# Optimization experiments

Measured on AMD Instinct MI355X. Metric: run time of the kernel, lower is better.

Reference implementation:

```python
import jax, jax.numpy as jnp
import numpy as np

EMBED = 1024
HEADS = 16
HEAD_DIM = EMBED // HEADS
SEQ = 2048
BATCH = 2


def setup_inputs() -> dict:
    key = jax.random.key(0)
    ks = jax.random.split(key, 5)
    s = 1.0 / np.sqrt(EMBED)
    return {
        "x": jax.random.normal(ks[0], (BATCH, SEQ, EMBED), jnp.float32),
        "W_qkv": jax.random.uniform(ks[1], (EMBED, 3 * EMBED), jnp.float32, -s, s),
        "b_qkv": jax.random.uniform(ks[2], (3 * EMBED,), jnp.float32, -s, s),
        "W_out": jax.random.uniform(ks[3], (EMBED, EMBED), jnp.float32, -s, s),
        "b_out": jax.random.uniform(ks[4], (EMBED,), jnp.float32, -s, s),
    }


def reference(x, W_qkv, b_qkv, W_out, b_out):
    B, S, E = x.shape
    qkv = x @ W_qkv + b_qkv                      # [B,S,3E]
    q, k, v = jnp.split(qkv, 3, axis=-1)
    # [B,S,E] -> [B,H,S,D]
    def heads(t):
        return t.reshape(B, S, HEADS, HEAD_DIM).transpose(0, 2, 1, 3)
    q, k, v = heads(q), heads(k), heads(v)
    scores = jnp.einsum("bhid,bhjd->bhij", q, k) / np.sqrt(HEAD_DIM)  # [B,H,S,S]
    causal = jnp.tril(jnp.ones((S, S), bool))
    scores = jnp.where(causal[None, None], scores, -jnp.inf)
    probs = jax.nn.softmax(scores, axis=-1)
    out = jnp.einsum("bhij,bhjd->bhid", probs, v)  # [B,H,S,D]
    out = out.transpose(0, 2, 1, 3).reshape(B, S, E)
    return out @ W_out + b_out
```

## Files before the change

kernel.cpp:

```cpp
#include <hip/hip_runtime.h>
#include <hip/hip_bf16.h>
#include <cstdint>
#include <cstddef>


typedef unsigned short u16;
typedef __attribute__((ext_vector_type(8))) short short8;
typedef __attribute__((ext_vector_type(4))) short short4v;
typedef __attribute__((ext_vector_type(4))) float floatx4;

#define MFMA16(a, b, c) __builtin_amdgcn_mfma_f32_16x16x32_bf16((a), (b), (c), 0, 0, 0)

#if __has_builtin(__builtin_amdgcn_mfma_f32_16x16x16_bf16)
#define PV_MFMA(a, b, c) __builtin_amdgcn_mfma_f32_16x16x16_bf16((a), (b), (c), 0, 0, 0)
#elif __has_builtin(__builtin_amdgcn_mfma_f32_16x16x16bf16_1k)
#define PV_MFMA(a, b, c) __builtin_amdgcn_mfma_f32_16x16x16bf16_1k((a), (b), (c), 0, 0, 0)
#else
static __device__ __forceinline__ floatx4 pv_mfma_asm(short4v a, short4v b, floatx4 c) {
    asm volatile("v_mfma_f32_16x16x16_bf16 %0, %1, %2, %0" : "+v"(c) : "v"(a), "v"(b));
    return c;
}
#define PV_MFMA(a, b, c) pv_mfma_asm((a), (b), (c))
#endif

#if __has_builtin(__builtin_amdgcn_exp2f)
#define EXP2(x) __builtin_amdgcn_exp2f(x)
#else
#define EXP2(x) exp2f(x)
#endif

#define QSCALE 0.18033688011f

static __device__ __forceinline__ u16 f2b(float f) {
    union { float f; uint32_t u; } v; v.f = f;
    return (u16)((v.u + 0x7fffu + ((v.u >> 16) & 1u)) >> 16);
}

static __device__ __forceinline__ uint32_t pkbf(float lo, float hi) {
    union { float f; uint32_t u; } a, b; a.f = lo; b.f = hi;
    return __builtin_amdgcn_perm(b.u + 0x8000u, a.u + 0x8000u, 0x07060302u);
}

static __device__ __forceinline__ void async_cp16(const u16* g, u16* lds_wave_base) {
    __builtin_amdgcn_global_load_lds((__attribute__((address_space(1))) void*)g,
                                     (__attribute__((address_space(3))) void*)lds_wave_base,
                                     16, 0, 0);
}


__global__ __launch_bounds__(256) void k_prep(const float* __restrict__ x,
                                              const float* __restrict__ Wq,
                                              const float* __restrict__ Wo,
                                              u16* __restrict__ xb,
                                              u16* __restrict__ wqkvT,
                                              u16* __restrict__ woutT) {
    int bx = blockIdx.x, tid = threadIdx.x;
    if (bx < 2048) {
        int g = bx * 256 + tid;
        const float4* s = (const float4*)x + (size_t)g * 2;
        float4 f0 = s[0], f1 = s[1];
        uint4 r;
        r.x = pkbf(f0.x, f0.y);
        r.y = pkbf(f0.z, f0.w);
        r.z = pkbf(f1.x, f1.y);
        r.w = pkbf(f1.z, f1.w);
        *(uint4*)(xb + (size_t)g * 8) = r;
        return;
    }
    __shared__ float t[32][33];
    const float* src;
    u16* dst;
    int R, C, b;
    if (bx < 5120) { b = bx - 2048; src = Wq; dst = wqkvT; R = 1024; C = 3072; }
    else           { b = bx - 5120; src = Wo; dst = woutT; R = 1024; C = 1024; }
    int nbx = C >> 5;
    int yq = b / nbx, xq = b - yq * nbx;
    int c0 = xq * 32, r0 = yq * 32;
    int tx = tid & 31, ty = tid >> 5;
#pragma unroll
    for (int i = 0; i < 4; ++i)
        t[ty + i * 8][tx] = src[(size_t)(r0 + ty + i * 8) * C + c0 + tx];
    __syncthreads();
#pragma unroll
    for (int i = 0; i < 4; ++i)
        dst[(size_t)(c0 + ty + i * 8) * R + r0 + tx] = f2b(t[tx][ty + i * 8]);
}


__global__ __launch_bounds__(256, 3) void k_qkv_gemm(const u16* __restrict__ A,
                                                     const u16* __restrict__ Bt,
                                                     const float* __restrict__ bias,
                                                     u16* __restrict__ Qb,
                                                     u16* __restrict__ Kb,
                                                     u16* __restrict__ Vtb) {
    __shared__ __align__(16) u16 As[3][128 * 32];
    __shared__ __align__(16) u16 Bs[3][128 * 32];
    int tid = threadIdx.x;
    int w = tid >> 6, lane = tid & 63, quad = lane >> 4, l16 = lane & 15;
    int wm = w >> 1, wn = w & 1;
    int m0 = blockIdx.y * 128, n0 = blockIdx.x * 128;
    int wb = (tid & ~63) * 8;

    int ra0 = tid >> 2, ca0 = (tid & 3) * 8;
    int ra1 = (256 + tid) >> 2, ca1 = (tid & 3) * 8;
    const u16* A0 = &A[(size_t)(m0 + ra0) * 1024 + ca0];
    const u16* A1 = &A[(size_t)(m0 + ra1) * 1024 + ca1];
    const u16* B0 = &Bt[(size_t)(n0 + ra0) * 1024 + ca0];
    const u16* B1 = &Bt[(size_t)(n0 + ra1) * 1024 + ca1];

    auto stage = [&](int src_kt, int slot) {
        int ko = src_kt * 32;
        async_cp16(A0 + ko, &As[slot][wb]);
        async_cp16(A1 + ko, &As[slot][2048 + wb]);
        async_cp16(B0 + ko, &Bs[slot][wb]);
        async_cp16(B1 + ko, &Bs[slot][2048 + wb]);
    };

    floatx4 acc[4][4] = {};
    stage(0, 0);
    stage(1, 1);

    for (int kt = 0; kt < 32; ++kt) {
        asm volatile("s_waitcnt vmcnt(4)" ::: "memory");
        asm volatile("s_barrier" ::: "memory");
        int jn = kt + 2;
        stage(jn < 32 ? jn : 31, jn % 3);
        int s = kt % 3;
        short8 af[4], bf[4];
#pragma unroll
        for (int mt = 0; mt < 4; ++mt)
            af[mt] = *(const short8*)&As[s][(wm * 64 + mt * 16 + l16) * 32 + quad * 8];
#pragma unroll
        for (int nt = 0; nt < 4; ++nt)
            bf[nt] = *(const short8*)&Bs[s][(wn * 64 + nt * 16 + l16) * 32 + quad * 8];
#pragma unroll
        for (int mt = 0; mt < 4; ++mt)
#pragma unroll
            for (int nt = 0; nt < 4; ++nt)
                acc[mt][nt] = MFMA16(af[mt], bf[nt], acc[mt][nt]);
    }

    int region = n0 >> 10;
    if (region == 2) {
#pragma unroll
        for (int mt = 0; mt < 4; ++mt)
#pragma unroll
            for (int nt = 0; nt < 4; ++nt) {
                int n_abs = n0 + wn * 64 + nt * 16 + l16;
                int e = n_abs & 1023, h = e >> 6, d = e & 63;
                float vb = bias[n_abs];
                int mrow = m0 + wm * 64 + mt * 16 + quad * 4;
                int b = mrow >> 11, s0 = mrow & 2047;
                uint2 val;
                val.x = pkbf(acc[mt][nt][0] + vb, acc[mt][nt][1] + vb);
                val.y = pkbf(acc[mt][nt][2] + vb, acc[mt][nt][3] + vb);
                *(uint2*)&Vtb[((size_t)(b * 16 + h) * 64 + d) * 2048 + s0] = val;
            }
    } else {
        u16* dst = region == 0 ? Qb : Kb;
        float scl = region == 0 ? QSCALE : 1.0f;
#pragma unroll
        for (int mt = 0; mt < 4; ++mt)
#pragma unroll
            for (int nt = 0; nt < 4; ++nt)
#pragma unroll
                for (int r = 0; r < 4; ++r) {
                    int m_abs = m0 + wm * 64 + mt * 16 + quad * 4 + r;
                    int n_abs = n0 + wn * 64 + nt * 16 + l16;
                    float val = (acc[mt][nt][r] + bias[n_abs]) * scl;
                    int e = n_abs & 1023, h = e >> 6, d = e & 63;
                    int b = m_abs >> 11, s = m_abs & 2047;
                    dst[((size_t)(b * 16 + h) * 2048 + s) * 64 + d] = f2b(val);
                }
    }
}


__global__ __launch_bounds__(256, 4) void k_out_gemm(const u16* __restrict__ A,
                                                     const u16* __restrict__ Bt,
                                                     const float* __restrict__ bias,
                                                     float* __restrict__ out) {
    __shared__ __align__(16) u16 As[3][64 * 32];
    __shared__ __align__(16) u16 Bs[3][128 * 32];
    int tid = threadIdx.x;
    int w = tid >> 6, lane = tid & 63, quad = lane >> 4, l16 = lane & 15;
    int wm = w >> 1, wn = w & 1;
    int m0 = blockIdx.y * 64, n0 = blockIdx.x * 128;
    int wb = (tid & ~63) * 8;

    int ra0 = tid >> 2, ca0 = (tid & 3) * 8;
    int ra1 = (256 + tid) >> 2;
    const u16* A0 = &A[(size_t)(m0 + ra0) * 1024 + ca0];
    const u16* B0 = &Bt[(size_t)(n0 + ra0) * 1024 + ca0];
    const u16* B1 = &Bt[(size_t)(n0 + ra1) * 1024 + ca0];

    auto stage = [&](int src_kt, int slot) {
        int ko = src_kt * 32;
        async_cp16(A0 + ko, &As[slot][wb]);
        async_cp16(B0 + ko, &Bs[slot][wb]);
        async_cp16(B1 + ko, &Bs[slot][2048 + wb]);
    };

    floatx4 acc[2][4] = {};
    stage(0, 0);
    stage(1, 1);

    for (int kt = 0; kt < 32; ++kt) {
        asm volatile("s_waitcnt vmcnt(3)" ::: "memory");
        asm volatile("s_barrier" ::: "memory");
        int jn = kt + 2;
        stage(jn < 32 ? jn : 31, jn % 3);
        int s = kt % 3;
        short8 af[2], bf[4];
#pragma unroll
        for (int mt = 0; mt < 2; ++mt)
            af[mt] = *(const short8*)&As[s][(wm * 32 + mt * 16 + l16) * 32 + quad * 8];
#pragma unroll
        for (int nt = 0; nt < 4; ++nt)
            bf[nt] = *(const short8*)&Bs[s][(wn * 64 + nt * 16 + l16) * 32 + quad * 8];
#pragma unroll
        for (int mt = 0; mt < 2; ++mt)
#pragma unroll
            for (int nt = 0; nt < 4; ++nt)
                acc[mt][nt] = MFMA16(af[mt], bf[nt], acc[mt][nt]);
    }

#pragma unroll
    for (int mt = 0; mt < 2; ++mt)
#pragma unroll
        for (int nt = 0; nt < 4; ++nt)
#pragma unroll
            for (int r = 0; r < 4; ++r) {
                int m_abs = m0 + wm * 32 + mt * 16 + quad * 4 + r;
                int n_abs = n0 + wn * 64 + nt * 16 + l16;
                out[(size_t)m_abs * 1024 + n_abs] = acc[mt][nt][r] + bias[n_abs];
            }
}


__global__ __launch_bounds__(256, 2) void k_attn(const u16* __restrict__ Qb,
                                                 const u16* __restrict__ Kb,
                                                 const u16* __restrict__ Vtb,
                                                 u16* __restrict__ attnb) {
    __shared__ __align__(16) u16 KV[4][2][4096];
    int tid = threadIdx.x;
    int w = tid >> 6, lane = tid & 63, quad = lane >> 4, l16 = lane & 15;
    int L = blockIdx.x;
    int bh = ((L & 7) << 2) | ((L >> 3) & 3);
    int idx = (L >> 5) & 15;
    int pr = idx < 8 ? idx : 23 - idx;
    int qta = pr, qtb = 31 - pr;
    const u16* Qp = Qb + (size_t)bh * 131072;
    const u16* Kp = Kb + (size_t)bh * 131072;
    const u16* Vp = Vtb + (size_t)bh * 131072;
    int b = bh >> 4, h = bh & 15;

    int r0 = tid >> 3, c0 = ((tid & 7) ^ (r0 & 7)) * 8;
    int f1 = 256 + tid;
    int r1 = f1 >> 3, c1 = ((f1 & 7) ^ (r1 & 7)) * 8;
    int kOff0 = r0 * 64 + c0, kOff1 = r1 * 64 + c1;
    int vOff0 = r0 * 2048 + c0, vOff1 = r1 * 2048 + c1;
    int wb = (tid & ~63) * 8;

    int qrowa = qta * 64 + w * 16 + l16;
    int qrowb = qtb * 64 + w * 16 + l16;
    short8 qa0 = *(const short8*)&Qp[(size_t)qrowa * 64 + quad * 8];
    short8 qa1 = *(const short8*)&Qp[(size_t)qrowa * 64 + 32 + quad * 8];
    short8 qb0 = *(const short8*)&Qp[(size_t)qrowb * 64 + quad * 8];
    short8 qb1 = *(const short8*)&Qp[(size_t)qrowb * 64 + 32 + quad * 8];

    int n = qtb + 1;

    auto stage = [&](int j) {
        u16* Ks = (u16*)KV[j & 3][0];
        u16* Vs = (u16*)KV[j & 3][1];
        const u16* kp = Kp + (size_t)j * 4096;
        const u16* vp = Vp + (size_t)j * 64;
        async_cp16(kp + kOff0, Ks + wb);
        async_cp16(kp + kOff1, Ks + 2048 + wb);
        async_cp16(vp + vOff0, Vs + wb);
        async_cp16(vp + vOff1, Vs + 2048 + wb);
    };

    floatx4 accA[4] = {}, accB[4] = {};
    float ma = -__builtin_inff(), la = 0.f;
    float mb = -__builtin_inff(), lb = 0.f;
    int sw = l16 & 7;

    stage(0); stage(1); stage(2);

    for (int kt = 0; kt < n; ++kt) {
        asm volatile("s_waitcnt vmcnt(8)" ::: "memory");
        asm volatile("s_barrier" ::: "memory");
        {
            int jn = kt + 3;
            stage(jn < n ? jn : n - 1);
        }
        const u16* Ks = (const u16*)KV[kt & 3][0];
        const u16* Vs = (const u16*)KV[kt & 3][1];

        short8 kfa[4], kfb[4];
#pragma unroll
        for (int nt = 0; nt < 4; ++nt) {
            int rb = (nt * 16 + l16) * 8;
            kfa[nt] = *(const short8*)&Ks[(rb + (quad ^ sw)) * 8];
            kfb[nt] = *(const short8*)&Ks[(rb + ((4 + quad) ^ sw)) * 8];
        }
        short4v vf[4][4];
#pragma unroll
        for (int dt = 0; dt < 4; ++dt) {
            const char* rowb = (const char*)Vs + (dt * 16 + l16) * 128 + (quad & 1) * 8;
#pragma unroll
            for (int nt = 0; nt < 4; ++nt) {
                int chunk = nt * 2 + (quad >> 1);
                vf[nt][dt] = *(const short4v*)(rowb + ((chunk ^ sw) * 16));
            }
        }

        auto tile_step = [&](short8 qf0, short8 qf1, int qt_this, float& mr, float& lr,
                             floatx4* accO) {
            floatx4 sa[4] = {};
#pragma unroll
            for (int nt = 0; nt < 4; ++nt) {
                sa[nt] = MFMA16(kfa[nt], qf0, sa[nt]);
                sa[nt] = MFMA16(kfb[nt], qf1, sa[nt]);
            }
            if (kt == qt_this) {
                int q_abs = qt_this * 64 + w * 16 + l16;
#pragma unroll
                for (int nt = 0; nt < 4; ++nt)
#pragma unroll
                    for (int r = 0; r < 4; ++r)
                        if (kt * 64 + nt * 16 + quad * 4 + r > q_abs)
                            sa[nt][r] = -__builtin_inff();
            }
            float v = sa[0][0];
#pragma unroll
            for (int nt = 0; nt < 4; ++nt)
#pragma unroll
                for (int r = 0; r < 4; ++r) v = fmaxf(v, sa[nt][r]);
            v = fmaxf(v, __shfl_xor(v, 16));
            v = fmaxf(v, __shfl_xor(v, 32));
            float m_new = fmaxf(mr, v);
            float alpha = EXP2(mr - m_new);
            float p[4][4];
            float rs = 0.f;
#pragma unroll
            for (int nt = 0; nt < 4; ++nt)
#pragma unroll
                for (int r = 0; r < 4; ++r) {
                    float e = EXP2(sa[nt][r] - m_new);
                    p[nt][r] = e;
                    rs += e;
                }
            rs += __shfl_xor(rs, 16);
            rs += __shfl_xor(rs, 32);
            lr = lr * alpha + rs;
            mr = m_new;
#pragma unroll
            for (int dt = 0; dt < 4; ++dt)
#pragma unroll
                for (int r = 0; r < 4; ++r) accO[dt][r] *= alpha;
#pragma unroll
            for (int nt = 0; nt < 4; ++nt) {
                union { uint2 u; short4v s; } pf;
                pf.u.x = pkbf(p[nt][0], p[nt][1]);
                pf.u.y = pkbf(p[nt][2], p[nt][3]);
#pragma unroll
                for (int dt = 0; dt < 4; ++dt)
                    accO[dt] = PV_MFMA(vf[nt][dt], pf.s, accO[dt]);
            }
        };

        tile_step(qb0, qb1, qtb, mb, lb, accB);
        if (kt <= qta) tile_step(qa0, qa1, qta, ma, la, accA);
    }

    auto epilogue = [&](int qt_this, float lr, const floatx4* accO) {
        int q_abs = qt_this * 64 + w * 16 + l16;
        float inv = 1.f / lr;
        size_t base = ((size_t)(b * 2048 + q_abs)) * 1024 + h * 64;
#pragma unroll
        for (int dt = 0; dt < 4; ++dt) {
            uint2 val;
            val.x = pkbf(accO[dt][0] * inv, accO[dt][1] * inv);
            val.y = pkbf(accO[dt][2] * inv, accO[dt][3] * inv);
            *(uint2*)&attnb[base + dt * 16 + quad * 4] = val;
        }
    };
    epilogue(qta, la, accA);
    epilogue(qtb, lb, accB);
}


extern "C" void kernel_launch(void* const* d_in, const int* in_sizes, int n_in,
                              void* d_out, int out_size, void* d_ws, size_t ws_size,
                              hipStream_t stream) {
    const float* x     = (const float*)d_in[0];
    const float* W_qkv = (const float*)d_in[1];
    const float* b_qkv = (const float*)d_in[2];
    const float* W_out = (const float*)d_in[3];
    const float* b_out = (const float*)d_in[4];
    float* out = (float*)d_out;

    char* p = (char*)d_ws;
    u16* xb    = (u16*)p; p += (size_t)4096 * 1024 * 2;
    u16* wqkvT = (u16*)p; p += (size_t)3072 * 1024 * 2;
    u16* woutT = (u16*)p; p += (size_t)1024 * 1024 * 2;
    u16* Qb    = (u16*)p; p += (size_t)32 * 2048 * 64 * 2;
    u16* Kb    = (u16*)p; p += (size_t)32 * 2048 * 64 * 2;
    u16* Vtb   = (u16*)p; p += (size_t)32 * 64 * 2048 * 2;
    u16* attnb = xb;

    k_prep<<<6144, 256, 0, stream>>>(x, W_qkv, W_out, xb, wqkvT, woutT);
    k_qkv_gemm<<<dim3(24, 32), 256, 0, stream>>>(xb, wqkvT, b_qkv, Qb, Kb, Vtb);
    k_attn<<<512, 256, 0, stream>>>(Qb, Kb, Vtb, attnb);
    k_out_gemm<<<dim3(8, 64), 256, 0, stream>>>(attnb, woutT, b_out, out);
}
```

Measured before the change: 179.8 us.

## Restructure attention kernel to 32x32x16 MFMA with per-wave query-tile roles

Each wave now owns a 32-row strip of a single query tile (A or B) instead of 16 rows of both tiles. It uses 32x32x16 bf16 MFMA for both QK^T and PV, reading K/V fragments straight from LDS inside the loop. The P fragments are rearranged across lane halves with shuffles so they can feed the PV MFMA. The accumulator rescale is skipped when no row max changes (ballot), and a block-parity flip alternates which waves take the short tile. The aim is fewer MFMA instructions, fewer LDS reads and less softmax bookkeeping per tile. The cost is load imbalance within a block: the waves on the short tile sit idle at barriers while the long-tile waves keep computing.

```diff
diff --git a/kernel.cpp b/kernel.cpp
--- a/kernel.cpp
+++ b/kernel.cpp
@@ -6,22 +6,11 @@
 
 typedef unsigned short u16;
 typedef __attribute__((ext_vector_type(8))) short short8;
-typedef __attribute__((ext_vector_type(4))) short short4v;
 typedef __attribute__((ext_vector_type(4))) float floatx4;
+typedef __attribute__((ext_vector_type(16))) float floatx16;
 
 #define MFMA16(a, b, c) __builtin_amdgcn_mfma_f32_16x16x32_bf16((a), (b), (c), 0, 0, 0)
-
-#if __has_builtin(__builtin_amdgcn_mfma_f32_16x16x16_bf16)
-#define PV_MFMA(a, b, c) __builtin_amdgcn_mfma_f32_16x16x16_bf16((a), (b), (c), 0, 0, 0)
-#elif __has_builtin(__builtin_amdgcn_mfma_f32_16x16x16bf16_1k)
-#define PV_MFMA(a, b, c) __builtin_amdgcn_mfma_f32_16x16x16bf16_1k((a), (b), (c), 0, 0, 0)
-#else
-static __device__ __forceinline__ floatx4 pv_mfma_asm(short4v a, short4v b, floatx4 c) {
-    asm volatile("v_mfma_f32_16x16x16_bf16 %0, %1, %2, %0" : "+v"(c) : "v"(a), "v"(b));
-    return c;
-}
-#define PV_MFMA(a, b, c) pv_mfma_asm((a), (b), (c))
-#endif
+#define MFMA32(a, b, c) __builtin_amdgcn_mfma_f32_32x32x16_bf16((a), (b), (c), 0, 0, 0)
 
 #if __has_builtin(__builtin_amdgcn_exp2f)
 #define EXP2(x) __builtin_amdgcn_exp2f(x)
@@ -30,6 +19,7 @@
 #endif
 
 #define QSCALE 0.18033688011f
+#define NEGINF (-__builtin_inff())
 
 static __device__ __forceinline__ u16 f2b(float f) {
     union { float f; uint32_t u; } v; v.f = f;
@@ -244,7 +234,8 @@
                                                  u16* __restrict__ attnb) {
     __shared__ __align__(16) u16 KV[4][2][4096];
     int tid = threadIdx.x;
-    int w = tid >> 6, lane = tid & 63, quad = lane >> 4, l16 = lane & 15;
+    int w = tid >> 6, lane = tid & 63;
+    int l31 = lane & 31, h5 = lane >> 5;
     int L = blockIdx.x;
     int bh = ((L & 7) << 2) | ((L >> 3) & 3);
     int idx = (L >> 5) & 15;
@@ -255,6 +246,12 @@
     const u16* Vp = Vtb + (size_t)bh * 131072;
     int b = bh >> 4, h = bh & 15;
 
+    int flip = (L >> 8) & 1;
+    int roleA = ((w >> 1) ^ flip) & 1;
+    int strip = w & 1;
+    int myqt = roleA ? qta : qtb;
+    int q_abs = myqt * 64 + strip * 32 + l31;
+
     int r0 = tid >> 3, c0 = ((tid & 7) ^ (r0 & 7)) * 8;
     int f1 = 256 + tid;
     int r1 = f1 >> 3, c1 = ((f1 & 7) ^ (r1 & 7)) * 8;
@@ -262,14 +259,13 @@
     int vOff0 = r0 * 2048 + c0, vOff1 = r1 * 2048 + c1;
     int wb = (tid & ~63) * 8;
 
-    int qrowa = qta * 64 + w * 16 + l16;
-    int qrowb = qtb * 64 + w * 16 + l16;
-    short8 qa0 = *(const short8*)&Qp[(size_t)qrowa * 64 + quad * 8];
-    short8 qa1 = *(const short8*)&Qp[(size_t)qrowa * 64 + 32 + quad * 8];
-    short8 qb0 = *(const short8*)&Qp[(size_t)qrowb * 64 + quad * 8];
-    short8 qb1 = *(const short8*)&Qp[(size_t)qrowb * 64 + 32 + quad * 8];
+    short8 qf[4];
+#pragma unroll
+    for (int ck = 0; ck < 4; ++ck)
+        qf[ck] = *(const short8*)&Qp[(size_t)q_abs * 64 + ck * 16 + h5 * 8];
 
     int n = qtb + 1;
+    int my_n = myqt + 1;
 
     auto stage = [&](int j) {
         u16* Ks = (u16*)KV[j & 3][0];
@@ -282,10 +278,8 @@
         async_cp16(vp + vOff1, Vs + 2048 + wb);
     };
 
-    floatx4 accA[4] = {}, accB[4] = {};
-    float ma = -__builtin_inff(), la = 0.f;
-    float mb = -__builtin_inff(), lb = 0.f;
-    int sw = l16 & 7;
+    floatx16 accO[2] = {};
+    float mr = NEGINF, lr = 0.f;
 
     stage(0); stage(1); stage(2);
 
@@ -296,100 +290,100 @@
             int jn = kt + 3;
             stage(jn < n ? jn : n - 1);
         }
-        const u16* Ks = (const u16*)KV[kt & 3][0];
-        const u16* Vs = (const u16*)KV[kt & 3][1];
-
-        short8 kfa[4], kfb[4];
-#pragma unroll
-        for (int nt = 0; nt < 4; ++nt) {
-            int rb = (nt * 16 + l16) * 8;
-            kfa[nt] = *(const short8*)&Ks[(rb + (quad ^ sw)) * 8];
-            kfb[nt] = *(const short8*)&Ks[(rb + ((4 + quad) ^ sw)) * 8];
-        }
-        short4v vf[4][4];
-#pragma unroll
-        for (int dt = 0; dt < 4; ++dt) {
-            const char* rowb = (const char*)Vs + (dt * 16 + l16) * 128 + (quad & 1) * 8;
-#pragma unroll
-            for (int nt = 0; nt < 4; ++nt) {
-                int chunk = nt * 2 + (quad >> 1);
-                vf[nt][dt] = *(const short4v*)(rowb + ((chunk ^ sw) * 16));
-            }
-        }
-
-        auto tile_step = [&](short8 qf0, short8 qf1, int qt_this, float& mr, float& lr,
-                             floatx4* accO) {
-            floatx4 sa[4] = {};
-#pragma unroll
-            for (int nt = 0; nt < 4; ++nt) {
-                sa[nt] = MFMA16(kfa[nt], qf0, sa[nt]);
-                sa[nt] = MFMA16(kfb[nt], qf1, sa[nt]);
-            }
-            if (kt == qt_this) {
-                int q_abs = qt_this * 64 + w * 16 + l16;
-#pragma unroll
-                for (int nt = 0; nt < 4; ++nt)
-#pragma unroll
-                    for (int r = 0; r < 4; ++r)
-                        if (kt * 64 + nt * 16 + quad * 4 + r > q_abs)
-                            sa[nt][r] = -__builtin_inff();
-            }
-            float v = sa[0][0];
-#pragma unroll
-            for (int nt = 0; nt < 4; ++nt)
-#pragma unroll
-                for (int r = 0; r < 4; ++r) v = fmaxf(v, sa[nt][r]);
-            v = fmaxf(v, __shfl_xor(v, 16));
-            v = fmaxf(v, __shfl_xor(v, 32));
-            float m_new = fmaxf(mr, v);
-            float alpha = EXP2(mr - m_new);
-            float p[4][4];
+        if (kt < my_n) {
+            const u16* Ks = (const u16*)KV[kt & 3][0];
+            const u16* Vs = (const u16*)KV[kt & 3][1];
+
+            floatx16 sa[2];
+            sa[0] = 0.f; sa[1] = 0.f;
+#pragma unroll
+            for (int kh = 0; kh < 2; ++kh) {
+                int row = kh * 32 + l31;
+                int swr = row & 7;
+#pragma unroll
+                for (int ck = 0; ck < 4; ++ck) {
+                    int cc = (ck * 2 + h5) ^ swr;
+                    short8 kf = *(const short8*)&Ks[row * 64 + cc * 8];
+                    sa[kh] = MFMA32(kf, qf[ck], sa[kh]);
+                }
+            }
+            if (kt == myqt) {
+#pragma unroll
+                for (int kh = 0; kh < 2; ++kh)
+#pragma unroll
+                    for (int rg = 0; rg < 16; ++rg) {
+                        int key = kt * 64 + kh * 32 + (rg & 3) + 8 * (rg >> 2) + 4 * h5;
+                        if (key > q_abs) sa[kh][rg] = NEGINF;
+                    }
+            }
+            float mx = NEGINF;
+#pragma unroll
+            for (int kh = 0; kh < 2; ++kh)
+#pragma unroll
+                for (int rg = 0; rg < 16; ++rg) mx = fmaxf(mx, sa[kh][rg]);
+            mx = fmaxf(mx, __shfl_xor(mx, 32));
+            float m_new = fmaxf(mr, mx);
+            if (__ballot(m_new > mr)) {
+                float alpha = EXP2(mr - m_new);
+                lr *= alpha;
+                accO[0] *= alpha;
+                accO[1] *= alpha;
+            }
+            mr = m_new;
+            float p[2][16];
             float rs = 0.f;
 #pragma unroll
-            for (int nt = 0; nt < 4; ++nt)
-#pragma unroll
-                for (int r = 0; r < 4; ++r) {
-                    float e = EXP2(sa[nt][r] - m_new);
-                    p[nt][r] = e;
+            for (int kh = 0; kh < 2; ++kh)
+#pragma unroll
+                for (int rg = 0; rg < 16; ++rg) {
+                    float e = EXP2(sa[kh][rg] - m_new);
+                    p[kh][rg] = e;
                     rs += e;
                 }
-            rs += __shfl_xor(rs, 16);
             rs += __shfl_xor(rs, 32);
-            lr = lr * alpha + rs;
-            mr = m_new;
-#pragma unroll
-            for (int dt = 0; dt < 4; ++dt)
-#pragma unroll
-                for (int r = 0; r < 4; ++r) accO[dt][r] *= alpha;
-#pragma unroll
-            for (int nt = 0; nt < 4; ++nt) {
-                union { uint2 u; short4v s; } pf;
-                pf.u.x = pkbf(p[nt][0], p[nt][1]);
-                pf.u.y = pkbf(p[nt][2], p[nt][3]);
-#pragma unroll
-                for (int dt = 0; dt < 4; ++dt)
-                    accO[dt] = PV_MFMA(vf[nt][dt], pf.s, accO[dt]);
-            }
-        };
-
-        tile_step(qb0, qb1, qtb, mb, lb, accB);
-        if (kt <= qta) tile_step(qa0, qa1, qta, ma, la, accA);
+            lr += rs;
+            uint32_t pk[2][8];
+#pragma unroll
+            for (int kh = 0; kh < 2; ++kh)
+#pragma unroll
+                for (int g = 0; g < 8; ++g)
+                    pk[kh][g] = pkbf(p[kh][2 * g], p[kh][2 * g + 1]);
+#pragma unroll
+            for (int kb = 0; kb < 4; ++kb) {
+                int hh = kb >> 1;
+                int base = 4 * (kb & 1);
+                uint32_t o0 = pk[hh][base + 2 * h5];
+                uint32_t o1 = pk[hh][base + 2 * h5 + 1];
+                uint32_t s0 = pk[hh][base + 2 * (1 - h5)];
+                uint32_t s1 = pk[hh][base + 2 * (1 - h5) + 1];
+                uint32_t e0 = (uint32_t)__shfl_xor((int)s0, 32);
+                uint32_t e1 = (uint32_t)__shfl_xor((int)s1, 32);
+                union { uint32_t u[4]; short8 v; } pf;
+                pf.u[0] = h5 ? e0 : o0;
+                pf.u[1] = h5 ? e1 : o1;
+                pf.u[2] = h5 ? o0 : e0;
+                pf.u[3] = h5 ? o1 : e1;
+#pragma unroll
+                for (int dh = 0; dh < 2; ++dh) {
+                    int vrow = dh * 32 + l31;
+                    int cc = (kb * 2 + h5) ^ (vrow & 7);
+                    short8 vf = *(const short8*)&Vs[vrow * 64 + cc * 8];
+                    accO[dh] = MFMA32(vf, pf.v, accO[dh]);
+                }
+            }
+        }
     }
 
-    auto epilogue = [&](int qt_this, float lr, const floatx4* accO) {
-        int q_abs = qt_this * 64 + w * 16 + l16;
-        float inv = 1.f / lr;
-        size_t base = ((size_t)(b * 2048 + q_abs)) * 1024 + h * 64;
-#pragma unroll
-        for (int dt = 0; dt < 4; ++dt) {
-            uint2 val;
-            val.x = pkbf(accO[dt][0] * inv, accO[dt][1] * inv);
-            val.y = pkbf(accO[dt][2] * inv, accO[dt][3] * inv);
-            *(uint2*)&attnb[base + dt * 16 + quad * 4] = val;
+    float inv = 1.f / lr;
+    size_t obase = ((size_t)(b * 2048 + q_abs)) * 1024 + h * 64;
+#pragma unroll
+    for (int dh = 0; dh < 2; ++dh)
+#pragma unroll
+        for (int g = 0; g < 8; ++g) {
+            int d0 = dh * 32 + 2 * (g & 1) + 8 * (g >> 1) + 4 * h5;
+            uint32_t v = pkbf(accO[dh][2 * g] * inv, accO[dh][2 * g + 1] * inv);
+            *(uint32_t*)&attnb[obase + d0] = v;
         }
-    };
-    epilogue(qta, la, accA);
-    epilogue(qtb, lb, accB);
 }
 
 
```

After: 227.2 us. 26.4% more time.

## Assign adjacent query tile pairs per attention block instead of mirrored pairs

Applied to the files above, without the earlier changes.

Each attention block now processes two adjacent 64-row query tiles (2*tile and 2*tile+1) instead of a mirrored pair (pr, 31-pr). Both query tiles share almost the same causal key/value range, so the block streams fewer K/V tiles per query tile and reuses each staged tile for two score computations. The trade-off is losing the load balance of the mirrored pairing: per-block work now grows linearly with the tile index, so the longest blocks do nearly twice the tile steps of the old balanced blocks.

```diff
diff --git a/kernel.cpp b/kernel.cpp
--- a/kernel.cpp
+++ b/kernel.cpp
@@ -30,6 +30,7 @@
 #endif
 
 #define QSCALE 0.18033688011f
+#define NEGINF (-__builtin_inff())
 
 static __device__ __forceinline__ u16 f2b(float f) {
     union { float f; uint32_t u; } v; v.f = f;
@@ -248,8 +249,7 @@
     int L = blockIdx.x;
     int bh = ((L & 7) << 2) | ((L >> 3) & 3);
     int idx = (L >> 5) & 15;
-    int pr = idx < 8 ? idx : 23 - idx;
-    int qta = pr, qtb = 31 - pr;
+    int tile = idx < 8 ? idx : 23 - idx;
     const u16* Qp = Qb + (size_t)bh * 131072;
     const u16* Kp = Kb + (size_t)bh * 131072;
     const u16* Vp = Vtb + (size_t)bh * 131072;
@@ -262,14 +262,14 @@
     int vOff0 = r0 * 2048 + c0, vOff1 = r1 * 2048 + c1;
     int wb = (tid & ~63) * 8;
 
-    int qrowa = qta * 64 + w * 16 + l16;
-    int qrowb = qtb * 64 + w * 16 + l16;
-    short8 qa0 = *(const short8*)&Qp[(size_t)qrowa * 64 + quad * 8];
-    short8 qa1 = *(const short8*)&Qp[(size_t)qrowa * 64 + 32 + quad * 8];
-    short8 qb0 = *(const short8*)&Qp[(size_t)qrowb * 64 + quad * 8];
-    short8 qb1 = *(const short8*)&Qp[(size_t)qrowb * 64 + 32 + quad * 8];
-
-    int n = qtb + 1;
+    int q_s0 = tile * 128 + w * 16 + l16;
+    int q_s1 = q_s0 + 64;
+    short8 q00 = *(const short8*)&Qp[(size_t)q_s0 * 64 + quad * 8];
+    short8 q01 = *(const short8*)&Qp[(size_t)q_s0 * 64 + 32 + quad * 8];
+    short8 q10 = *(const short8*)&Qp[(size_t)q_s1 * 64 + quad * 8];
+    short8 q11 = *(const short8*)&Qp[(size_t)q_s1 * 64 + 32 + quad * 8];
+
+    int n = 2 * tile + 2;
 
     auto stage = [&](int j) {
         u16* Ks = (u16*)KV[j & 3][0];
@@ -282,9 +282,9 @@
         async_cp16(vp + vOff1, Vs + 2048 + wb);
     };
 
-    floatx4 accA[4] = {}, accB[4] = {};
-    float ma = -__builtin_inff(), la = 0.f;
-    float mb = -__builtin_inff(), lb = 0.f;
+    floatx4 acc0[4] = {}, acc1[4] = {};
+    float m0 = NEGINF, l0 = 0.f;
+    float m1 = NEGINF, l1 = 0.f;
     int sw = l16 & 7;
 
     stage(0); stage(1); stage(2);
@@ -317,22 +317,21 @@
             }
         }
 
-        auto tile_step = [&](short8 qf0, short8 qf1, int qt_this, float& mr, float& lr,
-                             floatx4* accO) {
+        auto tile_step = [&](short8 qf0, short8 qf1, int q_abs, bool diag, float& mr,
+                             float& lr, floatx4* accO) {
             floatx4 sa[4] = {};
 #pragma unroll
             for (int nt = 0; nt < 4; ++nt) {
                 sa[nt] = MFMA16(kfa[nt], qf0, sa[nt]);
                 sa[nt] = MFMA16(kfb[nt], qf1, sa[nt]);
             }
-            if (kt == qt_this) {
-                int q_abs = qt_this * 64 + w * 16 + l16;
+            if (diag) {
 #pragma unroll
                 for (int nt = 0; nt < 4; ++nt)
 #pragma unroll
                     for (int r = 0; r < 4; ++r)
                         if (kt * 64 + nt * 16 + quad * 4 + r > q_abs)
-                            sa[nt][r] = -__builtin_inff();
+                            sa[nt][r] = NEGINF;
             }
             float v = sa[0][0];
 #pragma unroll
@@ -372,12 +371,12 @@
             }
         };
 
-        tile_step(qb0, qb1, qtb, mb, lb, accB);
-        if (kt <= qta) tile_step(qa0, qa1, qta, ma, la, accA);
+        tile_step(q10, q11, q_s1, kt == n - 1, m1, l1, acc1);
+        if (kt < n - 1)
+            tile_step(q00, q01, q_s0, kt == n - 2, m0, l0, acc0);
     }
 
-    auto epilogue = [&](int qt_this, float lr, const floatx4* accO) {
-        int q_abs = qt_this * 64 + w * 16 + l16;
+    auto epilogue = [&](int q_abs, float lr, const floatx4* accO) {
         float inv = 1.f / lr;
         size_t base = ((size_t)(b * 2048 + q_abs)) * 1024 + h * 64;
 #pragma unroll
@@ -388,8 +387,8 @@
             *(uint2*)&attnb[base + dt * 16 + quad * 4] = val;
         }
     };
-    epilogue(qta, la, accA);
-    epilogue(qtb, lb, accB);
+    epilogue(q_s0, l0, acc0);
+    epilogue(q_s1, l1, acc1);
 }
 
 
```

After: 177.3 us. No clear change (-1.4%).
